# Kernel optimization log

Measured on AMD Instinct MI355X. Metric: run time of the kernel, lower is better.

Reference implementation:

```python
import jax, jax.numpy as jnp
import numpy as np

MARGIN = 0.1
EPS = 1e-6
NUM_COMPARE = 5
N, D = 32768, 512


def setup_inputs() -> dict:
    key = jax.random.key(0)
    k1, k2 = jax.random.split(key)
    output = jax.random.normal(k1, (N, D), dtype=jnp.float32)
    target = jax.random.normal(k2, (N, D), dtype=jnp.float32)
    return {"output": output, "target": target}


def reference(output, target):
    # torch CosineSimilarity(dim=0, eps=1e-6): dot(x,y) / max(||x||*||y||, eps)
    n = output.shape[0]
    on = jnp.linalg.norm(output, axis=-1)          # [N]
    tn = jnp.linalg.norm(target, axis=-1)          # [N]
    # positive similarity: cos(target[i], output[i])
    pos = jnp.sum(output * target, axis=-1) / jnp.maximum(on * tn, EPS)  # [N]
    # negative similarities: cos(target[j], output[i]) for j in 0..NUM_COMPARE-1
    t5 = target[:NUM_COMPARE]                      # [5, D]
    tn5 = tn[:NUM_COMPARE]                         # [5]
    S = (output @ t5.T) / jnp.maximum(on[:, None] * tn5[None, :], EPS)   # [N, 5]
    # mask out j == i (only affects first NUM_COMPARE rows)
    i_idx = jnp.arange(n)[:, None]
    j_idx = jnp.arange(NUM_COMPARE)[None, :]
    mask = (i_idx != j_idx).astype(output.dtype)   # [N, 5]
    hinge = jax.nn.relu(MARGIN - pos[:, None] + S) * mask
    count = n * NUM_COMPARE - min(n, NUM_COMPARE)  # pairs with j != i
    return jnp.sum(hinge) / count
```

## Files before the change

kernel.cpp:

```cpp
#include <hip/hip_runtime.h>


constexpr int D   = 512;
constexpr int NC  = 5;
constexpr float MARGIN_F = 0.1f;
constexpr float EPS_F    = 1e-6f;

__global__ __launch_bounds__(256) void hinge_loss_kernel(
    const float* __restrict__ out, const float* __restrict__ tgt,
    float* __restrict__ result, int n, float inv_count)
{
  __shared__ float t5[NC * D];
  __shared__ float tt5[NC];
  __shared__ float block_sum;

  const int tid = threadIdx.x;
  if (tid == 0) block_sum = 0.f;

  for (int k = tid; k < NC * D / 4; k += 256) {
    reinterpret_cast<float4*>(t5)[k] = reinterpret_cast<const float4*>(tgt)[k];
  }
  __syncthreads();

  const int wid  = tid >> 6;
  const int lane = tid & 63;

  for (int j = wid; j < NC; j += 4) {
    float s = 0.f;
    for (int k = lane; k < D; k += 64) {
      const float v = t5[j * D + k];
      s = fmaf(v, v, s);
    }
    #pragma unroll
    for (int off = 32; off; off >>= 1) s += __shfl_xor(s, off);
    if (lane == 0) tt5[j] = s;
  }
  __syncthreads();

  float tn5[NC];
  #pragma unroll
  for (int j = 0; j < NC; ++j) tn5[j] = sqrtf(tt5[j]);

  float wave_sum = 0.f;

  const int stride = gridDim.x * 4;
  for (int i = blockIdx.x * 4 + wid; i < n; i += stride) {
    const float4* op = reinterpret_cast<const float4*>(out + (size_t)i * D);
    const float4* tp = reinterpret_cast<const float4*>(tgt + (size_t)i * D);
    float s_ot = 0.f, s_oo = 0.f, s_tt = 0.f;
    float s5[NC] = {0.f, 0.f, 0.f, 0.f, 0.f};
    #pragma unroll
    for (int c = 0; c < 2; ++c) {
      const float4 o = op[c * 64 + lane];
      const float4 t = tp[c * 64 + lane];
      s_ot += o.x * t.x + o.y * t.y + o.z * t.z + o.w * t.w;
      s_oo += o.x * o.x + o.y * o.y + o.z * o.z + o.w * o.w;
      s_tt += t.x * t.x + t.y * t.y + t.z * t.z + t.w * t.w;
      #pragma unroll
      for (int j = 0; j < NC; ++j) {
        const float4 v = reinterpret_cast<const float4*>(t5 + j * D)[c * 64 + lane];
        s5[j] += o.x * v.x + o.y * v.y + o.z * v.z + o.w * v.w;
      }
    }
    #pragma unroll
    for (int off = 32; off; off >>= 1) {
      s_ot += __shfl_xor(s_ot, off);
      s_oo += __shfl_xor(s_oo, off);
      s_tt += __shfl_xor(s_tt, off);
      #pragma unroll
      for (int j = 0; j < NC; ++j) s5[j] += __shfl_xor(s5[j], off);
    }
    if (lane == 0) {
      const float on  = sqrtf(s_oo);
      const float tn  = sqrtf(s_tt);
      const float pos = s_ot / fmaxf(on * tn, EPS_F);
      #pragma unroll
      for (int j = 0; j < NC; ++j) {
        const float S = s5[j] / fmaxf(on * tn5[j], EPS_F);
        const float h = fmaxf(0.f, MARGIN_F - pos + S);
        wave_sum += (i == j) ? 0.f : h;
      }
    }
  }

  if (lane == 0) atomicAdd(&block_sum, wave_sum);
  __syncthreads();
  if (tid == 0) atomicAdd(result, block_sum * inv_count);
}

extern "C" void kernel_launch(void* const* d_in, const int* in_sizes, int n_in,
                              void* d_out, int out_size, void* d_ws, size_t ws_size,
                              hipStream_t stream) {
  const float* out = (const float*)d_in[0];
  const float* tgt = (const float*)d_in[1];
  float* result = (float*)d_out;
  const int n = in_sizes[0] / D;
  const long long count = (long long)n * NC - (n < NC ? n : NC);
  const float inv_count = 1.0f / (float)count;

  hipMemsetAsync(d_out, 0, sizeof(float), stream);

  hinge_loss_kernel<<<2048, 256, 0, stream>>>(out, tgt, result, n, inv_count);
}
```

Measured before the change: 156.7 us.

## Split rows across 16-lane groups, read target rows via cache, two-pass reduction

Each wavefront now handles four rows at once, with 16 lanes per row. The five compare rows are read directly from global memory (through cache) instead of being staged in shared memory. Target norms are computed per wave without block syncs. The grid is sized to one row per lane group, and the shared-memory atomics plus the memset are replaced by per-wave partial sums and a second single-block reduce kernel. This removes the LDS staging and syncs and the atomic traffic, at the cost of an extra kernel launch and more cached global reads of the compare rows.

```diff
diff --git a/kernel.cpp b/kernel.cpp
--- a/kernel.cpp
+++ b/kernel.cpp
@@ -6,86 +6,94 @@
 constexpr float MARGIN_F = 0.1f;
 constexpr float EPS_F    = 1e-6f;
 
-__global__ __launch_bounds__(256) void hinge_loss_kernel(
+__global__ __launch_bounds__(256) void hinge_dots_kernel(
     const float* __restrict__ out, const float* __restrict__ tgt,
-    float* __restrict__ result, int n, float inv_count)
+    float* __restrict__ wave_partial, int n)
 {
-  __shared__ float t5[NC * D];
-  __shared__ float tt5[NC];
-  __shared__ float block_sum;
-
-  const int tid = threadIdx.x;
-  if (tid == 0) block_sum = 0.f;
-
-  for (int k = tid; k < NC * D / 4; k += 256) {
-    reinterpret_cast<float4*>(t5)[k] = reinterpret_cast<const float4*>(tgt)[k];
-  }
-  __syncthreads();
-
+  const int tid  = threadIdx.x;
   const int wid  = tid >> 6;
   const int lane = tid & 63;
+  const int sub  = lane & 15;
+  const int grp  = lane >> 4;
 
-  for (int j = wid; j < NC; j += 4) {
-    float s = 0.f;
-    for (int k = lane; k < D; k += 64) {
-      const float v = t5[j * D + k];
-      s = fmaf(v, v, s);
-    }
-    #pragma unroll
-    for (int off = 32; off; off >>= 1) s += __shfl_xor(s, off);
-    if (lane == 0) tt5[j] = s;
+  const float4* t5p = reinterpret_cast<const float4*>(tgt);
+
+  float sq_own = 0.f, sq_4 = 0.f;
+  #pragma unroll
+  for (int c = 0; c < 8; ++c) {
+    const float4 a = t5p[grp * 128 + c * 16 + sub];
+    const float4 b = t5p[4   * 128 + c * 16 + sub];
+    sq_own += a.x*a.x + a.y*a.y + a.z*a.z + a.w*a.w;
+    sq_4   += b.x*b.x + b.y*b.y + b.z*b.z + b.w*b.w;
   }
-  __syncthreads();
-
+  #pragma unroll
+  for (int off = 8; off; off >>= 1) {
+    sq_own += __shfl_xor(sq_own, off);
+    sq_4   += __shfl_xor(sq_4,   off);
+  }
   float tn5[NC];
   #pragma unroll
-  for (int j = 0; j < NC; ++j) tn5[j] = sqrtf(tt5[j]);
+  for (int j = 0; j < 4; ++j) tn5[j] = sqrtf(__shfl(sq_own, j * 16 + sub));
+  tn5[4] = sqrtf(sq_4);
 
-  float wave_sum = 0.f;
-
-  const int stride = gridDim.x * 4;
-  for (int i = blockIdx.x * 4 + wid; i < n; i += stride) {
-    const float4* op = reinterpret_cast<const float4*>(out + (size_t)i * D);
-    const float4* tp = reinterpret_cast<const float4*>(tgt + (size_t)i * D);
+  const int gwave = blockIdx.x * 4 + wid;
+  const int row   = gwave * 4 + grp;
+  float acc = 0.f;
+  if (row < n) {
+    const float4* op = reinterpret_cast<const float4*>(out) + (size_t)row * 128;
+    const float4* tp = reinterpret_cast<const float4*>(tgt) + (size_t)row * 128;
     float s_ot = 0.f, s_oo = 0.f, s_tt = 0.f;
     float s5[NC] = {0.f, 0.f, 0.f, 0.f, 0.f};
     #pragma unroll
-    for (int c = 0; c < 2; ++c) {
-      const float4 o = op[c * 64 + lane];
-      const float4 t = tp[c * 64 + lane];
-      s_ot += o.x * t.x + o.y * t.y + o.z * t.z + o.w * t.w;
-      s_oo += o.x * o.x + o.y * o.y + o.z * o.z + o.w * o.w;
-      s_tt += t.x * t.x + t.y * t.y + t.z * t.z + t.w * t.w;
+    for (int c = 0; c < 8; ++c) {
+      const float4 o = op[c * 16 + sub];
+      const float4 t = tp[c * 16 + sub];
+      s_ot += o.x*t.x + o.y*t.y + o.z*t.z + o.w*t.w;
+      s_oo += o.x*o.x + o.y*o.y + o.z*o.z + o.w*o.w;
+      s_tt += t.x*t.x + t.y*t.y + t.z*t.z + t.w*t.w;
       #pragma unroll
       for (int j = 0; j < NC; ++j) {
-        const float4 v = reinterpret_cast<const float4*>(t5 + j * D)[c * 64 + lane];
-        s5[j] += o.x * v.x + o.y * v.y + o.z * v.z + o.w * v.w;
+        const float4 v = t5p[j * 128 + c * 16 + sub];
+        s5[j] += o.x*v.x + o.y*v.y + o.z*v.z + o.w*v.w;
       }
     }
     #pragma unroll
-    for (int off = 32; off; off >>= 1) {
+    for (int off = 8; off; off >>= 1) {
       s_ot += __shfl_xor(s_ot, off);
       s_oo += __shfl_xor(s_oo, off);
       s_tt += __shfl_xor(s_tt, off);
       #pragma unroll
       for (int j = 0; j < NC; ++j) s5[j] += __shfl_xor(s5[j], off);
     }
-    if (lane == 0) {
-      const float on  = sqrtf(s_oo);
-      const float tn  = sqrtf(s_tt);
-      const float pos = s_ot / fmaxf(on * tn, EPS_F);
-      #pragma unroll
-      for (int j = 0; j < NC; ++j) {
-        const float S = s5[j] / fmaxf(on * tn5[j], EPS_F);
-        const float h = fmaxf(0.f, MARGIN_F - pos + S);
-        wave_sum += (i == j) ? 0.f : h;
-      }
+    const float on  = sqrtf(s_oo);
+    const float tn  = sqrtf(s_tt);
+    const float pos = s_ot / fmaxf(on * tn, EPS_F);
+    float h = 0.f;
+    #pragma unroll
+    for (int j = 0; j < NC; ++j) {
+      const float S = s5[j] / fmaxf(on * tn5[j], EPS_F);
+      const float hv = fmaxf(0.f, MARGIN_F - pos + S);
+      h += (row == j) ? 0.f : hv;
     }
+    acc = (sub == 0) ? h : 0.f;
   }
+  acc += __shfl_xor(acc, 16);
+  acc += __shfl_xor(acc, 32);
+  if (lane == 0) wave_partial[gwave] = acc;
+}
 
-  if (lane == 0) atomicAdd(&block_sum, wave_sum);
+__global__ __launch_bounds__(256) void reduce_kernel(
+    const float* __restrict__ part, float* __restrict__ result,
+    int nw, float inv_count)
+{
+  float s = 0.f;
+  for (int i = threadIdx.x; i < nw; i += 256) s += part[i];
+  #pragma unroll
+  for (int off = 32; off; off >>= 1) s += __shfl_xor(s, off);
+  __shared__ float ws[4];
+  if ((threadIdx.x & 63) == 0) ws[threadIdx.x >> 6] = s;
   __syncthreads();
-  if (tid == 0) atomicAdd(result, block_sum * inv_count);
+  if (threadIdx.x == 0) result[0] = (ws[0] + ws[1] + ws[2] + ws[3]) * inv_count;
 }
 
 extern "C" void kernel_launch(void* const* d_in, const int* in_sizes, int n_in,
@@ -94,11 +102,14 @@
   const float* out = (const float*)d_in[0];
   const float* tgt = (const float*)d_in[1];
   float* result = (float*)d_out;
+  float* partials = (float*)d_ws;
+
   const int n = in_sizes[0] / D;
+  const int blocks = (n + 15) / 16;
+  const int nwaves = blocks * 4;
   const long long count = (long long)n * NC - (n < NC ? n : NC);
   const float inv_count = 1.0f / (float)count;
 
-  hipMemsetAsync(d_out, 0, sizeof(float), stream);
-
-  hinge_loss_kernel<<<2048, 256, 0, stream>>>(out, tgt, result, n, inv_count);
+  hinge_dots_kernel<<<blocks, 256, 0, stream>>>(out, tgt, partials, n);
+  reduce_kernel<<<1, 256, 0, stream>>>(partials, result, nwaves, inv_count);
 }
```

Result: no change. 154.4 us (-1.5%).
